# Kernel tuning notes

Hardware: AMD Instinct MI355X
Metric: run time of the kernel (lower is better)

Reference implementation:

```python
import jax, jax.numpy as jnp
import numpy as np

B, CIN, T = 64, 64, 4096
F, K = 128, 64


def setup_inputs() -> dict:
    key = jax.random.key(0)
    k1, k2, k3, k4, k5 = jax.random.split(key, 5)
    x = jax.random.normal(k1, (B, CIN, T), dtype=jnp.float32)
    conv_weights = jax.random.normal(k2, (F, K), dtype=jnp.float32) * 0.2
    spat_weights = jax.random.normal(k3, (F, CIN), dtype=jnp.float32) * 0.2
    weight = jax.random.normal(k4, (F,), dtype=jnp.float32)
    bias = jax.random.normal(k5, (F,), dtype=jnp.float32)
    return {"x": x, "conv_weights": conv_weights, "spat_weights": spat_weights,
            "weight": weight, "bias": bias}


def reference(x, conv_weights, spat_weights, weight, bias):
    n_filters, ksize = conv_weights.shape
    n_in = spat_weights.shape[1]
    # rank-1 merged kernel: [F, Cin, K]
    merged = conv_weights[:, None, :] * spat_weights[:, :, None]
    # valid conv1d: x [B,Cin,T] -> conved [B,F,T-K+1]
    conved = jax.lax.conv_general_dilated(
        x, merged, window_strides=(1,), padding='VALID',
        dimension_numbers=('NCH', 'OIH', 'NCH'))
    # per-filter weight norm
    norm_w = jnp.sqrt(jnp.sum(merged * merged, axis=(1, 2)))  # [F]
    # input norm: sliding-window sum of x^2 over channels and window
    sq = jnp.sum(x * x, axis=1, keepdims=True)  # [B,1,T]
    ones_k = jnp.ones((1, 1, ksize), dtype=x.dtype)
    slide = jax.lax.conv_general_dilated(
        sq, ones_k, window_strides=(1,), padding='VALID',
        dimension_numbers=('NCH', 'OIH', 'NCH'))[:, 0, :]  # [B,Tout]
    norm_inputs = jnp.sqrt(slide)
    scale = np.sqrt(n_in * ksize).astype(np.float32)
    cos_sims = conved / (norm_w[None, :, None] * norm_inputs[:, None, :]) * scale
    mean_cos = jnp.mean(jnp.abs(cos_sims), axis=2)  # [B,F]
    out_per_wave = mean_cos * weight[None, :] + bias[None, :]
    return jnp.sum(out_per_wave, axis=1)  # [B]
```

## Files before the change

### kernel.cpp

```cpp
#include <hip/hip_runtime.h>
#include <hip/hip_bf16.h>
#include <cstdint>
#include <cstddef>

#define BB   64
#define CINN 64
#define TS   4096
#define FF   128
#define KS   64
#define TOUT (TS - KS + 1)
#define TT   2048
#define FGZ  8
#define SEG  (TT + KS)
#define SEG2 2432
#define YDW  (SEG2 / 2)
#define YLDSW (YDW + (YDW / 32) * 4)

#define TPB   256
#define SXT   37
#define SYB   68

typedef __attribute__((ext_vector_type(8))) short short8;
typedef __attribute__((ext_vector_type(4))) float f32x4;
union FragU { unsigned int u[4]; short8 v; uint4 q4; };

static __device__ __forceinline__ unsigned int f2bf_u(float f) {
    __hip_bfloat16 h = __float2bfloat16(f);
    return (unsigned int)*reinterpret_cast<unsigned short*>(&h);
}

__device__ __forceinline__ int swz(int p) { return p + ((p >> 5) << 2); }

__global__ __launch_bounds__(256) void k_spatial_mfma(
    const float* __restrict__ x, const float* __restrict__ sw,
    __hip_bfloat16* __restrict__ y, float* __restrict__ sq)
{
    __shared__ unsigned int xTd[TPB * SXT];
    __shared__ float ybuf[4 * 32 * SYB];
    __shared__ float sqred[4 * TPB];
    const int tid = threadIdx.x;
    const int b = blockIdx.y;
    const int t0 = blockIdx.x * TPB;

    {
        const int tj = tid & 63;
        const int cg = tid >> 6;
        float4 s4 = {0.f, 0.f, 0.f, 0.f};
#pragma unroll
        for (int i = 0; i < 8; ++i) {
            int cp = cg * 8 + i;
            const float* xr = x + ((size_t)b * CINN + 2 * cp) * TS + t0 + 4 * tj;
            float4 v0 = *(const float4*)xr;
            float4 v1 = *(const float4*)(xr + TS);
            s4.x += v0.x * v0.x + v1.x * v1.x;
            s4.y += v0.y * v0.y + v1.y * v1.y;
            s4.z += v0.z * v0.z + v1.z * v1.z;
            s4.w += v0.w * v0.w + v1.w * v1.w;
            xTd[(4 * tj + 0) * SXT + cp] = f2bf_u(v0.x) | (f2bf_u(v1.x) << 16);
            xTd[(4 * tj + 1) * SXT + cp] = f2bf_u(v0.y) | (f2bf_u(v1.y) << 16);
            xTd[(4 * tj + 2) * SXT + cp] = f2bf_u(v0.z) | (f2bf_u(v1.z) << 16);
            xTd[(4 * tj + 3) * SXT + cp] = f2bf_u(v0.w) | (f2bf_u(v1.w) << 16);
        }
        *(float4*)(sqred + cg * TPB + 4 * tj) = s4;
    }
    __syncthreads();
    if (tid < 64) {
        float4 a0 = *(const float4*)(sqred + 4 * tid);
        float4 a1 = *(const float4*)(sqred + TPB + 4 * tid);
        float4 a2 = *(const float4*)(sqred + 2 * TPB + 4 * tid);
        float4 a3 = *(const float4*)(sqred + 3 * TPB + 4 * tid);
        float4 s; s.x = a0.x + a1.x + a2.x + a3.x; s.y = a0.y + a1.y + a2.y + a3.y;
        s.z = a0.z + a1.z + a2.z + a3.z; s.w = a0.w + a1.w + a2.w + a3.w;
        *(float4*)(sq + (size_t)b * TS + t0 + 4 * tid) = s;
    }

    const int w  = tid >> 6;
    const int ln = tid & 63;
    const int m  = ln & 15;
    const int q  = ln >> 4;
    const int fbase = 32 * w;

    short8 Afr[2][2];
#pragma unroll
    for (int p = 0; p < 2; ++p)
#pragma unroll
        for (int s = 0; s < 2; ++s) {
            const float* swr = sw + (size_t)(fbase + 16 * p + m) * CINN + s * 32 + q * 8;
            float4 w0 = *(const float4*)swr;
            float4 w1 = *(const float4*)(swr + 4);
            FragU fa;
            fa.u[0] = f2bf_u(w0.x) | (f2bf_u(w0.y) << 16);
            fa.u[1] = f2bf_u(w0.z) | (f2bf_u(w0.w) << 16);
            fa.u[2] = f2bf_u(w1.x) | (f2bf_u(w1.y) << 16);
            fa.u[3] = f2bf_u(w1.z) | (f2bf_u(w1.w) << 16);
            Afr[p][s] = fa.v;
        }

    const int baseB = m * SXT + q * 4;
    float* yb = ybuf + w * (32 * SYB);

#pragma unroll
    for (int strip = 0; strip < 4; ++strip) {
#pragma unroll
        for (int tti = 0; tti < 4; ++tti) {
            const int tt = strip * 4 + tti;
            const int ad = baseB + tt * (16 * SXT);
            FragU b0, b1;
#pragma unroll
            for (int i = 0; i < 4; ++i) { b0.u[i] = xTd[ad + i]; b1.u[i] = xTd[ad + 16 + i]; }
            f32x4 acc0 = {0.f, 0.f, 0.f, 0.f};
            f32x4 acc1 = {0.f, 0.f, 0.f, 0.f};
            acc0 = __builtin_amdgcn_mfma_f32_16x16x32_bf16(Afr[0][0], b0.v, acc0, 0, 0, 0);
            acc0 = __builtin_amdgcn_mfma_f32_16x16x32_bf16(Afr[0][1], b1.v, acc0, 0, 0, 0);
            acc1 = __builtin_amdgcn_mfma_f32_16x16x32_bf16(Afr[1][0], b0.v, acc1, 0, 0, 0);
            acc1 = __builtin_amdgcn_mfma_f32_16x16x32_bf16(Afr[1][1], b1.v, acc1, 0, 0, 0);
            const int tl = tti * 16 + m;
#pragma unroll
            for (int r = 0; r < 4; ++r) {
                yb[(4 * q + r) * SYB + tl]      = acc0[r];
                yb[(16 + 4 * q + r) * SYB + tl] = acc1[r];
            }
        }
#pragma unroll
        for (int pr = 0; pr < 8; ++pr) {
            const int fl = pr * 4 + q;
            float4 v = *(const float4*)(yb + fl * SYB + 4 * m);
            uint2 o;
            o.x = f2bf_u(v.x) | (f2bf_u(v.y) << 16);
            o.y = f2bf_u(v.z) | (f2bf_u(v.w) << 16);
            *(uint2*)(y + ((size_t)b * FF + fbase + fl) * TS + t0 + strip * 64 + 4 * m) = o;
        }
    }
}

__global__ __launch_bounds__(256) void k_temporal_mfma(
    const __hip_bfloat16* __restrict__ y, const float* __restrict__ sq,
    const float* __restrict__ cw, const float* __restrict__ sw,
    const float* __restrict__ weight, const float* __restrict__ bias,
    float* __restrict__ out)
{
    __shared__ unsigned int ydb[2][YLDSW];
    __shared__ float rbuf[SEG];
    __shared__ float cwp[2][112];
    __shared__ float wn[FGZ];
    __shared__ float wred[4];
    const int tid = threadIdx.x;
    const int ln  = tid & 63;
    const int w   = tid >> 6;
    const int n   = ln & 15;
    const int q   = ln >> 4;
    const int b   = blockIdx.y;
    const int t0  = blockIdx.x * TT;
    const int f0  = blockIdx.z * FGZ;

    const float* sqrow = sq + (size_t)b * TS;
#pragma unroll
    for (int it = 0; it < 3; ++it) {
        int j = tid + 256 * it;
        if (j < SEG / 4) {
            int p = t0 + 4 * j; if (p > TS - 4) p = TS - 4;
            *(float4*)(rbuf + 4 * j) = *(const float4*)(sqrow + p);
        }
    }
    if (tid < 112) {
        float v = 0.f; int ci = tid - 15;
        if (ci >= 0 && ci < KS) v = cw[(size_t)f0 * KS + ci];
        cwp[0][tid] = v;
    }
    if (tid < FGZ) {
        int f = f0 + tid;
        float ssw = 0.f, scw = 0.f;
        for (int c = 0; c < CINN; ++c) { float v = sw[(size_t)f * CINN + c]; ssw += v * v; }
        for (int k = 0; k < KS; ++k)   { float v = cw[(size_t)f * KS + k];  scw += v * v; }
        wn[tid] = weight[f] * rsqrtf(ssw * scw) * (64.0f / (float)TOUT);
    }
    uint2 u0, u1, u2;
    {
        const uint2* r = (const uint2*)(y + ((size_t)b * FF + f0) * TS);
        int gg;
        gg = t0 / 4 + tid;       if (gg > TS / 4 - 1) gg = TS / 4 - 1; u0 = r[gg];
        gg = t0 / 4 + tid + 256; if (gg > TS / 4 - 1) gg = TS / 4 - 1; u1 = r[gg];
        if (tid < SEG2 / 4 - 512) {
            gg = t0 / 4 + tid + 512; if (gg > TS / 4 - 1) gg = TS / 4 - 1; u2 = r[gg];
        }
    }
    __syncthreads();

    const int base = 8 * tid;
    float rv[8];
    {
        float hd[8], tl[8];
        float s = 0.f;
#pragma unroll
        for (int mm = 0; mm < 16; ++mm) {
            float4 v = *(const float4*)(rbuf + base + 4 * mm);
            if (mm < 2) { hd[4 * mm] = v.x; hd[4 * mm + 1] = v.y; hd[4 * mm + 2] = v.z; hd[4 * mm + 3] = v.w; }
            s += (v.x + v.y) + (v.z + v.w);
        }
        float4 ta = *(const float4*)(rbuf + base + 64);
        float4 tb = *(const float4*)(rbuf + base + 68);
        tl[0] = ta.x; tl[1] = ta.y; tl[2] = ta.z; tl[3] = ta.w;
        tl[4] = tb.x; tl[5] = tb.y; tl[6] = tb.z; tl[7] = tb.w;
#pragma unroll
        for (int j = 0; j < 8; ++j) {
            int tpos = t0 + base + j;
            rv[j] = (tpos < TOUT) ? rsqrtf(s) : 0.f;
            s += tl[j] - hd[j];
        }
    }
    *(uint2*)(ydb[0] + swz(2 * tid))         = u0;
    *(uint2*)(ydb[0] + swz(2 * (tid + 256))) = u1;
    if (tid < SEG2 / 4 - 512) *(uint2*)(ydb[0] + swz(2 * (tid + 512))) = u2;
    if (1 < FGZ) {
        const uint2* r = (const uint2*)(y + ((size_t)b * FF + f0 + 1) * TS);
        int gg;
        gg = t0 / 4 + tid;       if (gg > TS / 4 - 1) gg = TS / 4 - 1; u0 = r[gg];
        gg = t0 / 4 + tid + 256; if (gg > TS / 4 - 1) gg = TS / 4 - 1; u1 = r[gg];
        if (tid < SEG2 / 4 - 512) {
            gg = t0 / 4 + tid + 512; if (gg > TS / 4 - 1) gg = TS / 4 - 1; u2 = r[gg];
        }
    }
    __syncthreads();
#pragma unroll
    for (int j = 0; j < 8; ++j) {
        int tl = base + j;
        int nn = tl & 15, mr = (tl >> 4) & 15, tile = tl >> 8;
        rbuf[tile * 256 + ((mr >> 2) * 16 + nn) * 4 + (mr & 3)] = rv[j];
    }
    __syncthreads();

    float acc = 0.f;
    for (int fi = 0; fi < FGZ; ++fi) {
        const int buf = fi & 1;
        if (fi + 1 < FGZ) {
            *(uint2*)(ydb[buf ^ 1] + swz(2 * tid))         = u0;
            *(uint2*)(ydb[buf ^ 1] + swz(2 * (tid + 256))) = u1;
            if (tid < SEG2 / 4 - 512) *(uint2*)(ydb[buf ^ 1] + swz(2 * (tid + 512))) = u2;
            if (tid >= 144 && tid < 144 + 112) {
                int u = tid - 144; float v = 0.f; int ci = u - 15;
                if (ci >= 0 && ci < KS) v = cw[(size_t)(f0 + fi + 1) * KS + ci];
                cwp[buf ^ 1][u] = v;
            }
            if (fi + 2 < FGZ) {
                const uint2* r = (const uint2*)(y + ((size_t)b * FF + f0 + fi + 2) * TS);
                int gg;
                gg = t0 / 4 + tid;       if (gg > TS / 4 - 1) gg = TS / 4 - 1; u0 = r[gg];
                gg = t0 / 4 + tid + 256; if (gg > TS / 4 - 1) gg = TS / 4 - 1; u1 = r[gg];
                if (tid < SEG2 / 4 - 512) {
                    gg = t0 / 4 + tid + 512; if (gg > TS / 4 - 1) gg = TS / 4 - 1; u2 = r[gg];
                }
            }
        }
        short8 Bf[3];
#pragma unroll
        for (int s = 0; s < 3; ++s) {
            const int off = 15 + 32 * s + 8 * q - n;
            FragU fb;
#pragma unroll
            for (int i = 0; i < 4; ++i)
                fb.u[i] = f2bf_u(cwp[buf][off + 2 * i]) | (f2bf_u(cwp[buf][off + 2 * i + 1]) << 16);
            Bf[s] = fb.v;
        }
        float facc = 0.f;
#pragma unroll
        for (int ti = 0; ti < 2; ++ti) {
            const int tile = 2 * w + ti;
            f32x4 d = {0.f, 0.f, 0.f, 0.f};
#pragma unroll
            for (int s = 0; s < 3; ++s) {
                FragU fa;
                fa.q4 = *(const uint4*)(ydb[buf] + swz(tile * 128 + 8 * n + 16 * s + 4 * q));
                d = __builtin_amdgcn_mfma_f32_16x16x32_bf16(fa.v, Bf[s], d, 0, 0, 0);
            }
            float4 r4 = *(const float4*)(rbuf + tile * 256 + 4 * ln);
            float rr[4]; *(float4*)rr = r4;
#pragma unroll
            for (int r = 0; r < 4; ++r) facc += fabsf(d[r]) * rr[r];
        }
        acc += wn[fi] * facc;
        __syncthreads();
    }

    for (int off = 32; off > 0; off >>= 1) acc += __shfl_down(acc, off, 64);
    if ((tid & 63) == 0) wred[tid >> 6] = acc;
    __syncthreads();
    if (tid == 0) atomicAdd(out + b, wred[0] + wred[1] + wred[2] + wred[3]);
    if (blockIdx.x == 0 && blockIdx.z == 0 && tid < FF) {
        float v = bias[tid];
        for (int off = 32; off > 0; off >>= 1) v += __shfl_down(v, off, 64);
        if ((tid & 63) == 0) atomicAdd(out + b, v);
    }
}

__global__ __launch_bounds__(256) void k_naive(
    const float* __restrict__ x, const float* __restrict__ cw,
    const float* __restrict__ sw, const float* __restrict__ weight,
    const float* __restrict__ bias, float* __restrict__ out)
{
    __shared__ float yl[TS];
    __shared__ float ql[TS];
    __shared__ float wred[4];
    const int f = blockIdx.x, b = blockIdx.y, tid = threadIdx.x;
    for (int t = tid; t < TS; t += 256) {
        float a = 0.f, s = 0.f;
        for (int c = 0; c < CINN; ++c) {
            float v = x[((size_t)b * CINN + c) * TS + t];
            a += sw[(size_t)f * CINN + c] * v;
            s += v * v;
        }
        yl[t] = a; ql[t] = s;
    }
    __syncthreads();
    float acc = 0.f;
    for (int t = tid; t < TOUT; t += 256) {
        float cv = 0.f, sl = 0.f;
        for (int k = 0; k < KS; ++k) { cv += cw[(size_t)f * KS + k] * yl[t + k]; sl += ql[t + k]; }
        acc += fabsf(cv) * rsqrtf(sl);
    }
    float ssw = 0.f, scw = 0.f;
    for (int c = 0; c < CINN; ++c) { float v = sw[(size_t)f * CINN + c]; ssw += v * v; }
    for (int k = 0; k < KS; ++k)   { float v = cw[(size_t)f * KS + k];  scw += v * v; }
    const float wnf = weight[f] * rsqrtf(ssw * scw) * 64.0f / (float)TOUT;
    for (int off = 32; off > 0; off >>= 1) acc += __shfl_down(acc, off, 64);
    if ((tid & 63) == 0) wred[tid >> 6] = acc;
    __syncthreads();
    if (tid == 0) {
        float tot = (wred[0] + wred[1] + wred[2] + wred[3]) * wnf;
        if (f == 0) {
            float bsum = 0.f;
            for (int ff = 0; ff < FF; ++ff) bsum += bias[ff];
            tot += bsum;
        }
        atomicAdd(out + b, tot);
    }
}

extern "C" void kernel_launch(void* const* d_in, const int* in_sizes, int n_in,
                              void* d_out, int out_size, void* d_ws, size_t ws_size,
                              hipStream_t stream) {
    const float* x  = (const float*)d_in[0];
    const float* cw = (const float*)d_in[1];
    const float* sw = (const float*)d_in[2];
    const float* w  = (const float*)d_in[3];
    const float* bs = (const float*)d_in[4];
    float* out = (float*)d_out;

    hipMemsetAsync(d_out, 0, (size_t)out_size * sizeof(float), stream);

    const size_t yBytes  = (size_t)BB * FF * TS * sizeof(__hip_bfloat16);
    const size_t sqBytes = (size_t)BB * TS * sizeof(float);

    if (yBytes + sqBytes <= ws_size) {
        __hip_bfloat16* ybf = (__hip_bfloat16*)d_ws;
        float* sq = (float*)((char*)d_ws + yBytes);
        k_spatial_mfma <<<dim3(TS / TPB, BB), 256, 0, stream>>>(x, sw, ybf, sq);
        k_temporal_mfma<<<dim3(TS / TT, BB, FF / FGZ), 256, 0, stream>>>(ybf, sq, cw, sw, w, bs, out);
    } else {
        k_naive<<<dim3(FF, BB), 256, 0, stream>>>(x, cw, sw, w, bs, out);
    }
}
```

Before: 145.7 us.

## Load temporal MFMA operands directly from global and precompute banded weight fragments

The temporal kernel stops staging the bf16 intermediate through double-buffered LDS with per-filter barriers. Instead, each lane loads its A fragments straight from global memory. A new small kernel builds the banded conv-weight B fragments and the per-filter norm scale once, and the temporal kernel reads them, which removes the in-loop bf16 conversions and the redundant norm computation. This trades LDS traffic and synchronisation for overlapping, uncoalesced-ish global/L2 reads, and it adds a padded tail region plus an extra launch and memset.

```diff
diff --git a/kernel.cpp b/kernel.cpp
--- a/kernel.cpp
+++ b/kernel.cpp
@@ -12,9 +12,6 @@
 #define TT   2048
 #define FGZ  8
 #define SEG  (TT + KS)
-#define SEG2 2432
-#define YDW  (SEG2 / 2)
-#define YLDSW (YDW + (YDW / 32) * 4)
 
 #define TPB   256
 #define SXT   37
@@ -29,7 +26,31 @@
     return (unsigned int)*reinterpret_cast<unsigned short*>(&h);
 }
 
-__device__ __forceinline__ int swz(int p) { return p + ((p >> 5) << 2); }
+__global__ void k_band(const float* __restrict__ cw, const float* __restrict__ sw,
+                       const float* __restrict__ weight,
+                       uint4* __restrict__ bandB, float* __restrict__ wnf) {
+    const int f = blockIdx.x, l = threadIdx.x;
+    const int n = l & 15, q = l >> 4;
+    for (int s = 0; s < 3; ++s) {
+        FragU o;
+#pragma unroll
+        for (int i = 0; i < 4; ++i) {
+            int i0 = 32 * s + 8 * q + 2 * i - n;
+            int i1 = i0 + 1;
+            float a = (i0 >= 0 && i0 < KS) ? cw[(size_t)f * KS + i0] : 0.f;
+            float c = (i1 >= 0 && i1 < KS) ? cw[(size_t)f * KS + i1] : 0.f;
+            o.u[i] = f2bf_u(a) | (f2bf_u(c) << 16);
+        }
+        bandB[((size_t)f * 3 + s) * 64 + l] = o.q4;
+    }
+    float a = sw[(size_t)f * CINN + l], c = cw[(size_t)f * KS + l];
+    float v = a * a, u = c * c;
+    for (int off = 32; off > 0; off >>= 1) {
+        v += __shfl_down(v, off, 64);
+        u += __shfl_down(u, off, 64);
+    }
+    if (l == 0) wnf[f] = weight[f] * rsqrtf(v * u) * (64.0f / (float)TOUT);
+}
 
 __global__ __launch_bounds__(256) void k_spatial_mfma(
     const float* __restrict__ x, const float* __restrict__ sw,
@@ -133,25 +154,19 @@
     }
 }
 
-__global__ __launch_bounds__(256) void k_temporal_mfma(
+__global__ __launch_bounds__(256) void k_temporal_direct(
     const __hip_bfloat16* __restrict__ y, const float* __restrict__ sq,
-    const float* __restrict__ cw, const float* __restrict__ sw,
-    const float* __restrict__ weight, const float* __restrict__ bias,
-    float* __restrict__ out)
+    const uint4* __restrict__ bandB, const float* __restrict__ wnf,
+    const float* __restrict__ bias, float* __restrict__ out)
 {
-    __shared__ unsigned int ydb[2][YLDSW];
     __shared__ float rbuf[SEG];
-    __shared__ float cwp[2][112];
-    __shared__ float wn[FGZ];
     __shared__ float wred[4];
     const int tid = threadIdx.x;
-    const int ln  = tid & 63;
-    const int w   = tid >> 6;
-    const int n   = ln & 15;
-    const int q   = ln >> 4;
-    const int b   = blockIdx.y;
-    const int t0  = blockIdx.x * TT;
-    const int f0  = blockIdx.z * FGZ;
+    const int ln = tid & 63, w = tid >> 6;
+    const int m = ln & 15, q = ln >> 4;
+    const int b = blockIdx.y;
+    const int t0 = blockIdx.x * TT;
+    const int f0 = blockIdx.z * FGZ;
 
     const float* sqrow = sq + (size_t)b * TS;
 #pragma unroll
@@ -162,28 +177,6 @@
             *(float4*)(rbuf + 4 * j) = *(const float4*)(sqrow + p);
         }
     }
-    if (tid < 112) {
-        float v = 0.f; int ci = tid - 15;
-        if (ci >= 0 && ci < KS) v = cw[(size_t)f0 * KS + ci];
-        cwp[0][tid] = v;
-    }
-    if (tid < FGZ) {
-        int f = f0 + tid;
-        float ssw = 0.f, scw = 0.f;
-        for (int c = 0; c < CINN; ++c) { float v = sw[(size_t)f * CINN + c]; ssw += v * v; }
-        for (int k = 0; k < KS; ++k)   { float v = cw[(size_t)f * KS + k];  scw += v * v; }
-        wn[tid] = weight[f] * rsqrtf(ssw * scw) * (64.0f / (float)TOUT);
-    }
-    uint2 u0, u1, u2;
-    {
-        const uint2* r = (const uint2*)(y + ((size_t)b * FF + f0) * TS);
-        int gg;
-        gg = t0 / 4 + tid;       if (gg > TS / 4 - 1) gg = TS / 4 - 1; u0 = r[gg];
-        gg = t0 / 4 + tid + 256; if (gg > TS / 4 - 1) gg = TS / 4 - 1; u1 = r[gg];
-        if (tid < SEG2 / 4 - 512) {
-            gg = t0 / 4 + tid + 512; if (gg > TS / 4 - 1) gg = TS / 4 - 1; u2 = r[gg];
-        }
-    }
     __syncthreads();
 
     const int base = 8 * tid;
@@ -208,18 +201,6 @@
             s += tl[j] - hd[j];
         }
     }
-    *(uint2*)(ydb[0] + swz(2 * tid))         = u0;
-    *(uint2*)(ydb[0] + swz(2 * (tid + 256))) = u1;
-    if (tid < SEG2 / 4 - 512) *(uint2*)(ydb[0] + swz(2 * (tid + 512))) = u2;
-    if (1 < FGZ) {
-        const uint2* r = (const uint2*)(y + ((size_t)b * FF + f0 + 1) * TS);
-        int gg;
-        gg = t0 / 4 + tid;       if (gg > TS / 4 - 1) gg = TS / 4 - 1; u0 = r[gg];
-        gg = t0 / 4 + tid + 256; if (gg > TS / 4 - 1) gg = TS / 4 - 1; u1 = r[gg];
-        if (tid < SEG2 / 4 - 512) {
-            gg = t0 / 4 + tid + 512; if (gg > TS / 4 - 1) gg = TS / 4 - 1; u2 = r[gg];
-        }
-    }
     __syncthreads();
 #pragma unroll
     for (int j = 0; j < 8; ++j) {
@@ -229,60 +210,35 @@
     }
     __syncthreads();
 
+    const __hip_bfloat16* ybase = y + ((size_t)b * FF + f0) * TS + t0 + 16 * m + 8 * q;
     float acc = 0.f;
     for (int fi = 0; fi < FGZ; ++fi) {
-        const int buf = fi & 1;
-        if (fi + 1 < FGZ) {
-            *(uint2*)(ydb[buf ^ 1] + swz(2 * tid))         = u0;
-            *(uint2*)(ydb[buf ^ 1] + swz(2 * (tid + 256))) = u1;
-            if (tid < SEG2 / 4 - 512) *(uint2*)(ydb[buf ^ 1] + swz(2 * (tid + 512))) = u2;
-            if (tid >= 144 && tid < 144 + 112) {
-                int u = tid - 144; float v = 0.f; int ci = u - 15;
-                if (ci >= 0 && ci < KS) v = cw[(size_t)(f0 + fi + 1) * KS + ci];
-                cwp[buf ^ 1][u] = v;
-            }
-            if (fi + 2 < FGZ) {
-                const uint2* r = (const uint2*)(y + ((size_t)b * FF + f0 + fi + 2) * TS);
-                int gg;
-                gg = t0 / 4 + tid;       if (gg > TS / 4 - 1) gg = TS / 4 - 1; u0 = r[gg];
-                gg = t0 / 4 + tid + 256; if (gg > TS / 4 - 1) gg = TS / 4 - 1; u1 = r[gg];
-                if (tid < SEG2 / 4 - 512) {
-                    gg = t0 / 4 + tid + 512; if (gg > TS / 4 - 1) gg = TS / 4 - 1; u2 = r[gg];
-                }
-            }
-        }
-        short8 Bf[3];
-#pragma unroll
-        for (int s = 0; s < 3; ++s) {
-            const int off = 15 + 32 * s + 8 * q - n;
-            FragU fb;
-#pragma unroll
-            for (int i = 0; i < 4; ++i)
-                fb.u[i] = f2bf_u(cwp[buf][off + 2 * i]) | (f2bf_u(cwp[buf][off + 2 * i + 1]) << 16);
-            Bf[s] = fb.v;
-        }
+        const uint4* bb = bandB + (size_t)(f0 + fi) * 3 * 64;
+        FragU B0, B1, B2;
+        B0.q4 = bb[ln]; B1.q4 = bb[64 + ln]; B2.q4 = bb[128 + ln];
+        const __hip_bfloat16* yr = ybase + (size_t)fi * TS;
         float facc = 0.f;
 #pragma unroll
         for (int ti = 0; ti < 2; ++ti) {
             const int tile = 2 * w + ti;
+            FragU a0, a1, a2;
+            a0.q4 = *(const uint4*)(yr + tile * 256);
+            a1.q4 = *(const uint4*)(yr + tile * 256 + 32);
+            a2.q4 = *(const uint4*)(yr + tile * 256 + 64);
             f32x4 d = {0.f, 0.f, 0.f, 0.f};
-#pragma unroll
-            for (int s = 0; s < 3; ++s) {
-                FragU fa;
-                fa.q4 = *(const uint4*)(ydb[buf] + swz(tile * 128 + 8 * n + 16 * s + 4 * q));
-                d = __builtin_amdgcn_mfma_f32_16x16x32_bf16(fa.v, Bf[s], d, 0, 0, 0);
-            }
+            d = __builtin_amdgcn_mfma_f32_16x16x32_bf16(a0.v, B0.v, d, 0, 0, 0);
+            d = __builtin_amdgcn_mfma_f32_16x16x32_bf16(a1.v, B1.v, d, 0, 0, 0);
+            d = __builtin_amdgcn_mfma_f32_16x16x32_bf16(a2.v, B2.v, d, 0, 0, 0);
             float4 r4 = *(const float4*)(rbuf + tile * 256 + 4 * ln);
             float rr[4]; *(float4*)rr = r4;
 #pragma unroll
             for (int r = 0; r < 4; ++r) facc += fabsf(d[r]) * rr[r];
         }
-        acc += wn[fi] * facc;
-        __syncthreads();
+        acc += wnf[f0 + fi] * facc;
     }
 
     for (int off = 32; off > 0; off >>= 1) acc += __shfl_down(acc, off, 64);
-    if ((tid & 63) == 0) wred[tid >> 6] = acc;
+    if (ln == 0) wred[w] = acc;
     __syncthreads();
     if (tid == 0) atomicAdd(out + b, wred[0] + wred[1] + wred[2] + wred[3]);
     if (blockIdx.x == 0 && blockIdx.z == 0 && tid < FF) {
@@ -347,14 +303,22 @@
 
     hipMemsetAsync(d_out, 0, (size_t)out_size * sizeof(float), stream);
 
-    const size_t yBytes  = (size_t)BB * FF * TS * sizeof(__hip_bfloat16);
-    const size_t sqBytes = (size_t)BB * TS * sizeof(float);
-
-    if (yBytes + sqBytes <= ws_size) {
+    const size_t yBytes    = (size_t)BB * FF * TS * sizeof(__hip_bfloat16);
+    const size_t padBytes  = 4096;
+    const size_t sqBytes   = (size_t)BB * TS * sizeof(float);
+    const size_t bandBytes = (size_t)FF * 3 * 64 * 16;
+    const size_t wnBytes   = (size_t)FF * sizeof(float);
+
+    if (yBytes + padBytes + sqBytes + bandBytes + wnBytes <= ws_size) {
         __hip_bfloat16* ybf = (__hip_bfloat16*)d_ws;
-        float* sq = (float*)((char*)d_ws + yBytes);
-        k_spatial_mfma <<<dim3(TS / TPB, BB), 256, 0, stream>>>(x, sw, ybf, sq);
-        k_temporal_mfma<<<dim3(TS / TT, BB, FF / FGZ), 256, 0, stream>>>(ybf, sq, cw, sw, w, bs, out);
+        char* p = (char*)d_ws + yBytes;
+        hipMemsetAsync(p, 0, padBytes, stream);
+        float* sq    = (float*)(p + padBytes);
+        uint4* bandB = (uint4*)(p + padBytes + sqBytes);
+        float* wnf   = (float*)(p + padBytes + sqBytes + bandBytes);
+        k_band<<<dim3(FF), 64, 0, stream>>>(cw, sw, w, bandB, wnf);
+        k_spatial_mfma  <<<dim3(TS / TPB, BB), 256, 0, stream>>>(x, sw, ybf, sq);
+        k_temporal_direct<<<dim3(TS / TT, BB, FF / FGZ), 256, 0, stream>>>(ybf, sq, bandB, wnf, bs, out);
     } else {
         k_naive<<<dim3(FF, BB), 256, 0, stream>>>(x, cw, sw, w, bs, out);
     }
```

After: 143.5 us. About the same (-1.5%).
